# Optimization experiments

Hardware: AMD Instinct MI355X
Metric: run time of the kernel (lower is better)

Reference implementation:

```python
import jax, jax.numpy as jnp
import numpy as np

N, F, B = 16384, 1024, 512


def setup_inputs() -> dict:
    key = jax.random.key(0)
    k1, k2, k3, k4, k5 = jax.random.split(key, 5)
    s = 1.0 / np.sqrt(F + B)
    return {
        "behavior": jax.random.normal(k1, (N, B), dtype=jnp.float32),
        "h_prev": jax.random.normal(k2, (N, F), dtype=jnp.float32),
        "c_prev": jax.random.normal(k3, (N, F), dtype=jnp.float32),
        "Wh": jax.random.normal(k4, (4 * F, F), dtype=jnp.float32) * s,
        "Wx": jax.random.normal(k5, (4 * F, B), dtype=jnp.float32) * s,
        "b": jnp.zeros((4 * F,), dtype=jnp.float32),
    }


def reference(behavior, h_prev, c_prev, Wh, Wx, b):
    # Fused single GEMM for all 4 gates: [n, 4F]
    gates = jnp.einsum("nf,gf->ng", h_prev, Wh) + jnp.einsum("nb,gb->ng", behavior, Wx) + b
    i, f, g, o = jnp.split(gates, 4, axis=-1)
    i = jax.nn.sigmoid(i)
    f = jax.nn.sigmoid(f)
    g = jnp.tanh(g)
    o = jax.nn.sigmoid(o)
    c = f * c_prev + i * g
    h = o * jnp.tanh(c)
    return h
```

## Files before the change

### kernel.cpp

```cpp
#include <hip/hip_runtime.h>
#include <hip/hip_bf16.h>
#include <stdint.h>
#include <type_traits>

#define N_ROWS 16384
#define F_DIM  1024
#define B_DIM  512
#define K_DIM  1536
#define G_DIM  4096
#define NT     24
#define CB_STR 68

typedef __bf16 v8bf __attribute__((ext_vector_type(8)));
typedef float  v4f  __attribute__((ext_vector_type(4)));

typedef const void __attribute__((address_space(1)))* gptr1;
typedef void       __attribute__((address_space(3)))* lptr3;

__device__ __forceinline__ unsigned short f2bf(float x) {
    union { float f; unsigned int u; } c; c.f = x;
    unsigned int u = c.u;
    return (unsigned short)((u + 0x7FFFu + ((u >> 16) & 1u)) >> 16);
}

__device__ __forceinline__ float sigmoidf_fast(float x) {
    return 1.f / (1.f + __expf(-x));
}
__device__ __forceinline__ float tanhf_fast(float x) {
    return 1.f - 2.f / (__expf(2.f * x) + 1.f);
}

__global__ void pack_all(const float* __restrict__ behavior,
                         const float* __restrict__ h_prev,
                         const float* __restrict__ Wh,
                         const float* __restrict__ Wx,
                         const float* __restrict__ b,
                         unsigned short* __restrict__ A,
                         unsigned short* __restrict__ W,
                         float* __restrict__ bperm) {
    const int blk = blockIdx.x;
    const int col = threadIdx.x * 8;
    const float* src;
    unsigned short* dst;
    if (blk < N_ROWS) {
        src = (col < F_DIM) ? h_prev + (long)blk * F_DIM + col
                            : behavior + (long)blk * B_DIM + (col - F_DIM);
        dst = A + (long)blk * K_DIM + col;
    } else {
        const int gp   = blk - N_ROWS;
        const int gate = gp & 3;
        const int f    = gp >> 2;
        const int g    = gate * F_DIM + f;
        src = (col < F_DIM) ? Wh + (long)g * F_DIM + col
                            : Wx + (long)g * B_DIM + (col - F_DIM);
        dst = W + (long)gp * K_DIM + col;
        if (threadIdx.x == 0) bperm[gp] = b[g];
    }
    float4 lo = *(const float4*)src;
    float4 hi = *(const float4*)(src + 4);
    union { unsigned short u[8]; int4 v; } p;
    p.u[0] = f2bf(lo.x); p.u[1] = f2bf(lo.y); p.u[2] = f2bf(lo.z); p.u[3] = f2bf(lo.w);
    p.u[4] = f2bf(hi.x); p.u[5] = f2bf(hi.y); p.u[6] = f2bf(hi.z); p.u[7] = f2bf(hi.w);
    *(int4*)dst = p.v;
}

__global__ __launch_bounds__(512, 2) void lstm_gemm(
    const unsigned short* __restrict__ A,
    const unsigned short* __restrict__ W,
    const float* __restrict__ bperm,
    const float* __restrict__ c_prev,
    float* __restrict__ out)
{
    extern __shared__ char smem[];

    const int bid = blockIdx.x;
    const int n0  = (bid & 15) << 8;
    const int m0  = (bid >> 4) << 8;

    const int tid  = threadIdx.x;
    const int lane = tid & 63;
    const int wave = tid >> 6;
    const int wmi  = wave >> 2;
    const int wni  = wave & 3;
    const int lrow = lane & 15;
    const int quad = lane >> 4;

    const int g7  = lrow & 7;
    const int cs0 = (quad ^ g7) << 4;
    const int cs1 = ((4 + quad) ^ g7) << 4;
    const int aRd = wmi * 16384 + lrow * 128;
    const int bRd = wni * 8192  + lrow * 128;

    const int srow = lane >> 3;
    const int schk = (lane & 7) ^ srow;
    const unsigned short* sA = A + (long)(m0 + wave * 8 + srow) * K_DIM + schk * 8;
    const unsigned short* sB = W + (long)(n0 + wave * 8 + srow) * K_DIM + schk * 8;
    const int sDst = wave * 1024;

    v4f acc[8][4] = {};

    auto stage4 = [&](const unsigned short* src, int ldsbase, int koff) {
#pragma unroll
        for (int u = 0; u < 4; ++u)
            __builtin_amdgcn_global_load_lds(
                (gptr1)(src + (long)u * 64 * K_DIM + koff),
                (lptr3)(smem + ldsbase + u * 8192 + sDst), 16, 0, 0);
    };

#define MFMA_BLK(MB)                                                            \
    __builtin_amdgcn_s_setprio(1);                                              \
    _Pragma("unroll")                                                           \
    for (int mt = 0; mt < 4; ++mt)                                              \
        _Pragma("unroll")                                                       \
        for (int nt = 0; nt < 4; ++nt)                                          \
            acc[(MB)*4 + mt][nt] = __builtin_amdgcn_mfma_f32_16x16x32_bf16(     \
                afr[mt], bfr[nt], acc[(MB)*4 + mt][nt], 0, 0, 0);               \
    __builtin_amdgcn_s_setprio(0);

    auto tile = [&](int BUF, int kn, auto pf_tag) {
        constexpr bool PF = decltype(pf_tag)::value;
        const int Ab = BUF * 32768;
        const int Bb = 65536 + Ab;
        const int Pb = (BUF ^ 1) * 32768;
        v8bf afr[4], bfr[4];

#pragma unroll
        for (int nt = 0; nt < 4; ++nt) bfr[nt] = *(const v8bf*)(smem + Bb + bRd + nt * 2048 + cs0);
#pragma unroll
        for (int mt = 0; mt < 4; ++mt) afr[mt] = *(const v8bf*)(smem + Ab + aRd + mt * 2048 + cs0);
        if constexpr (PF) stage4(sA, Pb, kn);
        __builtin_amdgcn_s_barrier();
        asm volatile("s_waitcnt lgkmcnt(0)" ::: "memory");
        MFMA_BLK(0)
        __builtin_amdgcn_s_barrier();

#pragma unroll
        for (int mt = 0; mt < 4; ++mt) afr[mt] = *(const v8bf*)(smem + Ab + aRd + (4 + mt) * 2048 + cs0);
        if constexpr (PF) stage4(sB, 65536 + Pb, kn);
        __builtin_amdgcn_s_barrier();
        asm volatile("s_waitcnt lgkmcnt(0)" ::: "memory");
        MFMA_BLK(1)
        __builtin_amdgcn_s_barrier();

#pragma unroll
        for (int nt = 0; nt < 4; ++nt) bfr[nt] = *(const v8bf*)(smem + Bb + bRd + nt * 2048 + cs1);
#pragma unroll
        for (int mt = 0; mt < 4; ++mt) afr[mt] = *(const v8bf*)(smem + Ab + aRd + mt * 2048 + cs1);
        __builtin_amdgcn_s_barrier();
        asm volatile("s_waitcnt lgkmcnt(0)" ::: "memory");
        MFMA_BLK(0)
        __builtin_amdgcn_s_barrier();

#pragma unroll
        for (int mt = 0; mt < 4; ++mt) afr[mt] = *(const v8bf*)(smem + Ab + aRd + (4 + mt) * 2048 + cs1);
        asm volatile("s_waitcnt vmcnt(0)" ::: "memory");
        __builtin_amdgcn_s_barrier();
        asm volatile("s_waitcnt lgkmcnt(0)" ::: "memory");
        MFMA_BLK(1)
        __builtin_amdgcn_s_barrier();
    };

    stage4(sA, 0, 0);
    stage4(sB, 65536, 0);
    asm volatile("s_waitcnt vmcnt(0)" ::: "memory");
    __builtin_amdgcn_s_barrier();

    int kn = 64;
    for (int t = 0; t < NT - 1; ++t) {
        tile(t & 1, kn, std::true_type{});
        kn += 64;
    }
    tile((NT - 1) & 1, 0, std::false_type{});
#undef MFMA_BLK

    float* cbuf = (float*)smem;
    const int fbase = n0 >> 2;
#pragma unroll
    for (int i = 0; i < 8; ++i) {
        const int q  = i * 512 + tid;
        const int r  = q >> 4;
        const int c4 = (q & 15) << 2;
        *(float4*)&cbuf[r * CB_STR + c4] =
            *(const float4*)&c_prev[(long)(m0 + r) * F_DIM + fbase + c4];
    }
    __syncthreads();

    const int l3 = lane & 3;
    const int fl = (lane >> 2) & 3;
#pragma unroll
    for (int nt = 0; nt < 4; ++nt) {
        const int   gcol = n0 + wni * 64 + nt * 16 + lrow;
        const float bias = bperm[gcol];
#pragma unroll
        for (int mt = 0; mt < 8; ++mt) {
            float a0 = acc[mt][nt][0] + bias;
            float a1 = acc[mt][nt][1] + bias;
            float a2 = acc[mt][nt][2] + bias;
            float a3 = acc[mt][nt][3] + bias;
            float s0 = (lane & 1) ? a0 : a1;
            float s1 = (lane & 1) ? a2 : a3;
            float t0 = __shfl_xor(s0, 1, 64);
            float t1 = __shfl_xor(s1, 1, 64);
            if (lane & 1) { a0 = t0; a2 = t1; } else { a1 = t0; a3 = t1; }
            s0 = (lane & 2) ? a0 : a2;
            s1 = (lane & 2) ? a1 : a3;
            t0 = __shfl_xor(s0, 2, 64);
            t1 = __shfl_xor(s1, 2, 64);
            if (lane & 2) { a0 = t0; a1 = t1; } else { a2 = t0; a3 = t1; }
            const float iv = sigmoidf_fast(a0);
            const float fv = sigmoidf_fast(a1);
            const float gv = tanhf_fast(a2);
            const float ov = sigmoidf_fast(a3);
            const int lr = wmi * 128 + mt * 16 + quad * 4 + l3;
            const int lc = wni * 16 + nt * 4 + fl;
            const float cp = cbuf[lr * CB_STR + lc];
            const float cv = fv * cp + iv * gv;
            cbuf[lr * CB_STR + lc] = ov * tanhf_fast(cv);
        }
    }
    __syncthreads();

#pragma unroll
    for (int i = 0; i < 8; ++i) {
        const int q  = i * 512 + tid;
        const int r  = q >> 4;
        const int c4 = (q & 15) << 2;
        *(float4*)&out[(long)(m0 + r) * F_DIM + fbase + c4] =
            *(const float4*)&cbuf[r * CB_STR + c4];
    }
}

extern "C" void kernel_launch(void* const* d_in, const int* in_sizes, int n_in,
                              void* d_out, int out_size, void* d_ws, size_t ws_size,
                              hipStream_t stream) {
    const float* behavior = (const float*)d_in[0];
    const float* h_prev   = (const float*)d_in[1];
    const float* c_prev   = (const float*)d_in[2];
    const float* Wh       = (const float*)d_in[3];
    const float* Wx       = (const float*)d_in[4];
    const float* b        = (const float*)d_in[5];
    float* out = (float*)d_out;

    unsigned short* A  = (unsigned short*)d_ws;
    unsigned short* W  = A + (size_t)N_ROWS * K_DIM;
    float*       bperm = (float*)(W + (size_t)G_DIM * K_DIM);

    hipFuncSetAttribute(reinterpret_cast<const void*>(lstm_gemm),
                        hipFuncAttributeMaxDynamicSharedMemorySize, 131072);

    pack_all<<<N_ROWS + G_DIM, 192, 0, stream>>>(behavior, h_prev, Wh, Wx, b, A, W, bperm);
    lstm_gemm<<<dim3((N_ROWS / 256) * (G_DIM / 256)), 512, 131072, stream>>>(A, W, bperm, c_prev, out);
}
```

Before: 418.8 us.

## Reorder GEMM k-loop into M-quarter phases with partial vmcnt waits

Restructures each k-tile so both K halves of B fragments are loaded once and A is processed in four M-quarters, each issuing two MFMAs per accumulator. Prefetch of the next tile is split into single-row loads spread across the four phases, with partial vmcnt waits instead of a full drain at tile end. The load order is arranged so that the first half of the next tile becomes available earlier. The aim is to overlap global-to-LDS traffic with compute and avoid the full vmcnt(0) stall. The cost is more register pressure for the B fragments and fragile wait counts tied to the issue order.

```diff
diff --git a/kernel.cpp b/kernel.cpp
--- a/kernel.cpp
+++ b/kernel.cpp
@@ -99,22 +99,29 @@
 
     v4f acc[8][4] = {};
 
-    auto stage4 = [&](const unsigned short* src, int ldsbase, int koff) {
-#pragma unroll
-        for (int u = 0; u < 4; ++u)
-            __builtin_amdgcn_global_load_lds(
-                (gptr1)(src + (long)u * 64 * K_DIM + koff),
-                (lptr3)(smem + ldsbase + u * 8192 + sDst), 16, 0, 0);
+    auto stage1 = [&](const unsigned short* src, int ldsbase, int u, int koff) {
+        __builtin_amdgcn_global_load_lds(
+            (gptr1)(src + (long)u * 64 * K_DIM + koff),
+            (lptr3)(smem + ldsbase + u * 8192 + sDst), 16, 0, 0);
     };
 
-#define MFMA_BLK(MB)                                                            \
+#define LOAD_A(Q)                                                               \
+    afr[0][0] = *(const v8bf*)(smem + Ab + aRd + (2*(Q)    ) * 2048 + cs0);     \
+    afr[0][1] = *(const v8bf*)(smem + Ab + aRd + (2*(Q)    ) * 2048 + cs1);     \
+    afr[1][0] = *(const v8bf*)(smem + Ab + aRd + (2*(Q) + 1) * 2048 + cs0);     \
+    afr[1][1] = *(const v8bf*)(smem + Ab + aRd + (2*(Q) + 1) * 2048 + cs1);
+
+#define MFMA_Q(Q)                                                               \
     __builtin_amdgcn_s_setprio(1);                                              \
     _Pragma("unroll")                                                           \
-    for (int mt = 0; mt < 4; ++mt)                                              \
+    for (int j = 0; j < 2; ++j)                                                 \
         _Pragma("unroll")                                                       \
-        for (int nt = 0; nt < 4; ++nt)                                          \
-            acc[(MB)*4 + mt][nt] = __builtin_amdgcn_mfma_f32_16x16x32_bf16(     \
-                afr[mt], bfr[nt], acc[(MB)*4 + mt][nt], 0, 0, 0);               \
+        for (int nt = 0; nt < 4; ++nt) {                                        \
+            acc[2*(Q)+j][nt] = __builtin_amdgcn_mfma_f32_16x16x32_bf16(         \
+                afr[j][0], bfr[nt][0], acc[2*(Q)+j][nt], 0, 0, 0);              \
+            acc[2*(Q)+j][nt] = __builtin_amdgcn_mfma_f32_16x16x32_bf16(         \
+                afr[j][1], bfr[nt][1], acc[2*(Q)+j][nt], 0, 0, 0);              \
+        }                                                                       \
     __builtin_amdgcn_s_setprio(0);
 
     auto tile = [&](int BUF, int kn, auto pf_tag) {
@@ -122,47 +129,55 @@
         const int Ab = BUF * 32768;
         const int Bb = 65536 + Ab;
         const int Pb = (BUF ^ 1) * 32768;
-        v8bf afr[4], bfr[4];
-
-#pragma unroll
-        for (int nt = 0; nt < 4; ++nt) bfr[nt] = *(const v8bf*)(smem + Bb + bRd + nt * 2048 + cs0);
-#pragma unroll
-        for (int mt = 0; mt < 4; ++mt) afr[mt] = *(const v8bf*)(smem + Ab + aRd + mt * 2048 + cs0);
-        if constexpr (PF) stage4(sA, Pb, kn);
-        __builtin_amdgcn_s_barrier();
-        asm volatile("s_waitcnt lgkmcnt(0)" ::: "memory");
-        MFMA_BLK(0)
-        __builtin_amdgcn_s_barrier();
-
-#pragma unroll
-        for (int mt = 0; mt < 4; ++mt) afr[mt] = *(const v8bf*)(smem + Ab + aRd + (4 + mt) * 2048 + cs0);
-        if constexpr (PF) stage4(sB, 65536 + Pb, kn);
-        __builtin_amdgcn_s_barrier();
-        asm volatile("s_waitcnt lgkmcnt(0)" ::: "memory");
-        MFMA_BLK(1)
-        __builtin_amdgcn_s_barrier();
-
-#pragma unroll
-        for (int nt = 0; nt < 4; ++nt) bfr[nt] = *(const v8bf*)(smem + Bb + bRd + nt * 2048 + cs1);
-#pragma unroll
-        for (int mt = 0; mt < 4; ++mt) afr[mt] = *(const v8bf*)(smem + Ab + aRd + mt * 2048 + cs1);
-        __builtin_amdgcn_s_barrier();
-        asm volatile("s_waitcnt lgkmcnt(0)" ::: "memory");
-        MFMA_BLK(0)
-        __builtin_amdgcn_s_barrier();
-
-#pragma unroll
-        for (int mt = 0; mt < 4; ++mt) afr[mt] = *(const v8bf*)(smem + Ab + aRd + (4 + mt) * 2048 + cs1);
-        asm volatile("s_waitcnt vmcnt(0)" ::: "memory");
-        __builtin_amdgcn_s_barrier();
-        asm volatile("s_waitcnt lgkmcnt(0)" ::: "memory");
-        MFMA_BLK(1)
+        v8bf afr[2][2], bfr[4][2];
+
+#pragma unroll
+        for (int nt = 0; nt < 4; ++nt) {
+            bfr[nt][0] = *(const v8bf*)(smem + Bb + bRd + nt * 2048 + cs0);
+            bfr[nt][1] = *(const v8bf*)(smem + Bb + bRd + nt * 2048 + cs1);
+        }
+        LOAD_A(0)
+        if constexpr (PF) { stage1(sB, 65536 + Pb, 0, kn); stage1(sB, 65536 + Pb, 1, kn); }
+        __builtin_amdgcn_s_barrier();
+        asm volatile("s_waitcnt lgkmcnt(0)" ::: "memory");
+        MFMA_Q(0)
+        __builtin_amdgcn_s_barrier();
+
+        LOAD_A(1)
+        if constexpr (PF) {
+            stage1(sB, 65536 + Pb, 2, kn); stage1(sB, 65536 + Pb, 3, kn);
+            asm volatile("s_waitcnt vmcnt(4)" ::: "memory");
+        } else {
+            asm volatile("s_waitcnt vmcnt(0)" ::: "memory");
+        }
+        __builtin_amdgcn_s_barrier();
+        asm volatile("s_waitcnt lgkmcnt(0)" ::: "memory");
+        MFMA_Q(1)
+        __builtin_amdgcn_s_barrier();
+
+        LOAD_A(2)
+        if constexpr (PF) { stage1(sA, Pb, 0, kn); stage1(sA, Pb, 2, kn); }
+        __builtin_amdgcn_s_barrier();
+        asm volatile("s_waitcnt lgkmcnt(0)" ::: "memory");
+        MFMA_Q(2)
+        __builtin_amdgcn_s_barrier();
+
+        LOAD_A(3)
+        if constexpr (PF) {
+            stage1(sA, Pb, 1, kn); stage1(sA, Pb, 3, kn);
+            asm volatile("s_waitcnt vmcnt(2)" ::: "memory");
+        }
+        __builtin_amdgcn_s_barrier();
+        asm volatile("s_waitcnt lgkmcnt(0)" ::: "memory");
+        MFMA_Q(3)
         __builtin_amdgcn_s_barrier();
     };
 
-    stage4(sA, 0, 0);
-    stage4(sB, 65536, 0);
-    asm volatile("s_waitcnt vmcnt(0)" ::: "memory");
+    stage1(sB, 65536, 0, 0); stage1(sB, 65536, 1, 0);
+    stage1(sB, 65536, 2, 0); stage1(sB, 65536, 3, 0);
+    stage1(sA, 0, 0, 0);     stage1(sA, 0, 2, 0);
+    stage1(sA, 0, 1, 0);     stage1(sA, 0, 3, 0);
+    asm volatile("s_waitcnt vmcnt(2)" ::: "memory");
     __builtin_amdgcn_s_barrier();
 
     int kn = 64;
@@ -171,7 +186,8 @@
         kn += 64;
     }
     tile((NT - 1) & 1, 0, std::false_type{});
-#undef MFMA_BLK
+#undef LOAD_A
+#undef MFMA_Q
 
     float* cbuf = (float*)smem;
     const int fbase = n0 >> 2;
```

New measurement: 430.3 us. 2.7% more time.

## Restructure GEMM K-tile loop: issue all prefetches upfront, drop intra-tile barriers

Applied to the files above, without the earlier changes.

Each K-tile now issues all eight global-to-LDS prefetch loads for the next buffer at the start, instead of splitting them across two phases. The four barrier-separated MFMA phases become a single loop over four M-quarters. B fragments for both K-halves are loaded once per tile, and A fragments are streamed per quarter. Only one vmcnt wait and one barrier remain at the end of the tile. The aim is to cut barrier stalls and let the compiler interleave LDS reads with MFMAs, at the cost of more live fragment registers and less explicit wave-level synchronisation.

```diff
diff --git a/kernel.cpp b/kernel.cpp
--- a/kernel.cpp
+++ b/kernel.cpp
@@ -99,69 +99,58 @@
 
     v4f acc[8][4] = {};
 
-    auto stage4 = [&](const unsigned short* src, int ldsbase, int koff) {
-#pragma unroll
-        for (int u = 0; u < 4; ++u)
-            __builtin_amdgcn_global_load_lds(
-                (gptr1)(src + (long)u * 64 * K_DIM + koff),
-                (lptr3)(smem + ldsbase + u * 8192 + sDst), 16, 0, 0);
+    auto stage1 = [&](const unsigned short* src, int ldsbase, int u, int koff) {
+        __builtin_amdgcn_global_load_lds(
+            (gptr1)(src + (long)u * 64 * K_DIM + koff),
+            (lptr3)(smem + ldsbase + u * 8192 + sDst), 16, 0, 0);
     };
-
-#define MFMA_BLK(MB)                                                            \
-    __builtin_amdgcn_s_setprio(1);                                              \
-    _Pragma("unroll")                                                           \
-    for (int mt = 0; mt < 4; ++mt)                                              \
-        _Pragma("unroll")                                                       \
-        for (int nt = 0; nt < 4; ++nt)                                          \
-            acc[(MB)*4 + mt][nt] = __builtin_amdgcn_mfma_f32_16x16x32_bf16(     \
-                afr[mt], bfr[nt], acc[(MB)*4 + mt][nt], 0, 0, 0);               \
-    __builtin_amdgcn_s_setprio(0);
 
     auto tile = [&](int BUF, int kn, auto pf_tag) {
         constexpr bool PF = decltype(pf_tag)::value;
         const int Ab = BUF * 32768;
         const int Bb = 65536 + Ab;
         const int Pb = (BUF ^ 1) * 32768;
-        v8bf afr[4], bfr[4];
-
-#pragma unroll
-        for (int nt = 0; nt < 4; ++nt) bfr[nt] = *(const v8bf*)(smem + Bb + bRd + nt * 2048 + cs0);
-#pragma unroll
-        for (int mt = 0; mt < 4; ++mt) afr[mt] = *(const v8bf*)(smem + Ab + aRd + mt * 2048 + cs0);
-        if constexpr (PF) stage4(sA, Pb, kn);
-        __builtin_amdgcn_s_barrier();
-        asm volatile("s_waitcnt lgkmcnt(0)" ::: "memory");
-        MFMA_BLK(0)
-        __builtin_amdgcn_s_barrier();
-
-#pragma unroll
-        for (int mt = 0; mt < 4; ++mt) afr[mt] = *(const v8bf*)(smem + Ab + aRd + (4 + mt) * 2048 + cs0);
-        if constexpr (PF) stage4(sB, 65536 + Pb, kn);
-        __builtin_amdgcn_s_barrier();
-        asm volatile("s_waitcnt lgkmcnt(0)" ::: "memory");
-        MFMA_BLK(1)
-        __builtin_amdgcn_s_barrier();
-
-#pragma unroll
-        for (int nt = 0; nt < 4; ++nt) bfr[nt] = *(const v8bf*)(smem + Bb + bRd + nt * 2048 + cs1);
-#pragma unroll
-        for (int mt = 0; mt < 4; ++mt) afr[mt] = *(const v8bf*)(smem + Ab + aRd + mt * 2048 + cs1);
-        __builtin_amdgcn_s_barrier();
-        asm volatile("s_waitcnt lgkmcnt(0)" ::: "memory");
-        MFMA_BLK(0)
-        __builtin_amdgcn_s_barrier();
-
-#pragma unroll
-        for (int mt = 0; mt < 4; ++mt) afr[mt] = *(const v8bf*)(smem + Ab + aRd + (4 + mt) * 2048 + cs1);
+        v8bf afr[2][2], bfr[4][2];
+
+        if constexpr (PF) {
+#pragma unroll
+            for (int u = 0; u < 4; ++u) stage1(sB, 65536 + Pb, u, kn);
+#pragma unroll
+            for (int u = 0; u < 4; ++u) stage1(sA, Pb, u, kn);
+        }
+
+#pragma unroll
+        for (int nt = 0; nt < 4; ++nt) {
+            bfr[nt][0] = *(const v8bf*)(smem + Bb + bRd + nt * 2048 + cs0);
+            bfr[nt][1] = *(const v8bf*)(smem + Bb + bRd + nt * 2048 + cs1);
+        }
+
+#pragma unroll
+        for (int Q = 0; Q < 4; ++Q) {
+            afr[0][0] = *(const v8bf*)(smem + Ab + aRd + (2*Q    ) * 2048 + cs0);
+            afr[0][1] = *(const v8bf*)(smem + Ab + aRd + (2*Q    ) * 2048 + cs1);
+            afr[1][0] = *(const v8bf*)(smem + Ab + aRd + (2*Q + 1) * 2048 + cs0);
+            afr[1][1] = *(const v8bf*)(smem + Ab + aRd + (2*Q + 1) * 2048 + cs1);
+            __builtin_amdgcn_s_setprio(1);
+#pragma unroll
+            for (int kh = 0; kh < 2; ++kh)
+#pragma unroll
+                for (int j = 0; j < 2; ++j)
+#pragma unroll
+                    for (int nt = 0; nt < 4; ++nt)
+                        acc[2*Q + j][nt] = __builtin_amdgcn_mfma_f32_16x16x32_bf16(
+                            afr[j][kh], bfr[nt][kh], acc[2*Q + j][nt], 0, 0, 0);
+            __builtin_amdgcn_s_setprio(0);
+        }
+
         asm volatile("s_waitcnt vmcnt(0)" ::: "memory");
         __builtin_amdgcn_s_barrier();
-        asm volatile("s_waitcnt lgkmcnt(0)" ::: "memory");
-        MFMA_BLK(1)
-        __builtin_amdgcn_s_barrier();
     };
 
-    stage4(sA, 0, 0);
-    stage4(sB, 65536, 0);
+#pragma unroll
+    for (int u = 0; u < 4; ++u) stage1(sB, 65536, u, 0);
+#pragma unroll
+    for (int u = 0; u < 4; ++u) stage1(sA, 0, u, 0);
     asm volatile("s_waitcnt vmcnt(0)" ::: "memory");
     __builtin_amdgcn_s_barrier();
 
@@ -171,7 +160,6 @@
         kn += 64;
     }
     tile((NT - 1) & 1, 0, std::false_type{});
-#undef MFMA_BLK
 
     float* cbuf = (float*)smem;
     const int fbase = n0 >> 2;
```

Result: no change. 423.2 us (+1.1%).
